# Performance work log

Hardware: AMD Instinct MI355X
Metric: run time of the kernel (lower is better)

Reference implementation:

```python
import jax, jax.numpy as jnp
import numpy as np

P = 100000   # num places
T = 100000   # num transitions
E = 400000   # edges per direction
H = 128      # hidden_dim
L = 3        # num_gnn_layers


def setup_inputs() -> dict:
    key = jax.random.key(0)
    ks = jax.random.split(key, 24)
    w = lambda i, sh: jax.random.normal(ks[i], sh, dtype=jnp.float32) * 0.02
    z = lambda sh: jnp.zeros(sh, dtype=jnp.float32)
    return {
        "place_features": jax.random.uniform(ks[0], (P,), dtype=jnp.float32),
        "transition_features": jax.random.normal(ks[1], (T, 8), dtype=jnp.float32),
        "prefix_encoding": jax.random.normal(ks[2], (18,), dtype=jnp.float32),
        # pre edges: place -> transition ; post edges: transition -> place
        "pre_edge_index": jnp.stack([jax.random.randint(ks[3], (E,), 0, P),
                                     jax.random.randint(ks[4], (E,), 0, T)]).astype(jnp.int32),
        "post_edge_index": jnp.stack([jax.random.randint(ks[5], (E,), 0, T),
                                      jax.random.randint(ks[6], (E,), 0, P)]).astype(jnp.int32),
        # embeddings
        "W_pe": w(7, (1, H)), "b_pe": z((H,)),
        "W_te": w(8, (8, H)), "b_te": z((H,)),
        "W_pr": w(9, (18, H)), "b_pr": z((H,)),
        # per-layer HeteroGraphConv params (stacked over L)
        "p2t_W": w(10, (L, H, H)), "p2t_b": z((L, H)),
        "t2p_W": w(11, (L, H, H)), "t2p_b": z((L, H)),
        "pu_W": w(12, (L, 2 * H, H)), "pu_b": z((L, H)),
        "tu_W": w(13, (L, 2 * H, H)), "tu_b": z((L, H)),
        "pa_W": w(14, (L, H)), "pa_b": z((L,)),
        "ta_W": w(15, (L, H)), "ta_b": z((L,)),
        # pooling + predictor head
        "W_pp": w(16, (H, H)), "b_pp": z((H,)),
        "W_tp": w(17, (H, H)), "b_tp": z((H,)),
        "W1": w(18, (3 * H, 2 * H)), "b1": z((2 * H,)),
        "W2": w(19, (2 * H, H)), "b2": z((H,)),
        "W3": w(20, (H, T)), "b3": z((T,)),
    }


def _forward(place_features, transition_features, prefix_encoding,
             W_pe, b_pe, W_te, b_te, W_pr, b_pr,
             p2t_W, p2t_b, t2p_W, t2p_b, pu_W, pu_b, tu_W, tu_b,
             pa_W, pa_b, ta_W, ta_b,
             W_pp, b_pp, W_tp, b_tp, W1, b1, W2, b2, W3, b3,
             pre_edge_index, post_edge_index):
    place_h = place_features[:, None] @ W_pe + b_pe            # [P,H]
    trans_h = transition_features @ W_te + b_te                # [T,H]
    prefix_h = prefix_encoding[None, :] @ W_pr + b_pr          # [1,H]
    p_src, p_dst = pre_edge_index[0], pre_edge_index[1]        # place idx, trans idx
    t_src, t_dst = post_edge_index[0], post_edge_index[1]      # trans idx, place idx
    nP, nT = place_h.shape[0], trans_h.shape[0]
    for l in range(L):  # fixed small layer count
        # place -> transition: gather, linear, softmax over ALL edges (dim=0 in torch), scatter-add
        m_pt = place_h[p_src] @ p2t_W[l] + p2t_b[l]            # [E,H]
        a_pt = jax.nn.softmax(m_pt @ ta_W[l] + ta_b[l], axis=0)  # [E]
        trans_msg = jax.ops.segment_sum(m_pt * a_pt[:, None], p_dst, num_segments=nT)
        # transition -> place
        m_tp = trans_h[t_src] @ t2p_W[l] + t2p_b[l]            # [E,H]
        a_tp = jax.nn.softmax(m_tp @ pa_W[l] + pa_b[l], axis=0)
        place_msg = jax.ops.segment_sum(m_tp * a_tp[:, None], t_dst, num_segments=nP)
        # residual update + relu (dropout is identity at eval)
        place_new = jnp.concatenate([place_h, place_msg], axis=1) @ pu_W[l] + pu_b[l]
        trans_new = jnp.concatenate([trans_h, trans_msg], axis=1) @ tu_W[l] + tu_b[l]
        place_h = jax.nn.relu(place_h + place_new)
        trans_h = jax.nn.relu(trans_h + trans_new)
    place_global = jnp.mean(place_h @ W_pp + b_pp, axis=0, keepdims=True)   # [1,H]
    trans_global = jnp.mean(trans_h @ W_tp + b_tp, axis=0, keepdims=True)   # [1,H]
    combined = jnp.concatenate([place_global, trans_global, prefix_h], axis=1)  # [1,3H]
    h1 = jax.nn.relu(combined @ W1 + b1)
    h2 = jax.nn.relu(h1 @ W2 + b2)
    logits = h2 @ W3 + b3                                      # [1,T]
    return jax.nn.sigmoid(logits)                              # predicted_transitions


def reference(place_features, transition_features, prefix_encoding,
              pre_edge_index, post_edge_index,
              W_pe, b_pe, W_te, b_te, W_pr, b_pr,
              p2t_W, p2t_b, t2p_W, t2p_b, pu_W, pu_b, tu_W, tu_b,
              pa_W, pa_b, ta_W, ta_b,
              W_pp, b_pp, W_tp, b_tp, W1, b1, W2, b2, W3, b3):
    return _forward(place_features, transition_features, prefix_encoding,
                    W_pe, b_pe, W_te, b_te, W_pr, b_pr,
                    p2t_W, p2t_b, t2p_W, t2p_b, pu_W, pu_b, tu_W, tu_b,
                    pa_W, pa_b, ta_W, ta_b,
                    W_pp, b_pp, W_tp, b_tp, W1, b1, W2, b2, W3, b3,
                    pre_edge_index, post_edge_index)
```

## Files before the change

### kernel.cpp

```cpp
#include <hip/hip_runtime.h>
#include <cstddef>

#define H 128

typedef unsigned short ushort_t;
typedef unsigned char uchar_t;
typedef __attribute__((ext_vector_type(8))) short short8;
typedef __attribute__((ext_vector_type(4))) float floatx4;
typedef __attribute__((ext_vector_type(2))) float floatx2;

__device__ __forceinline__ unsigned fkey(float f){
    unsigned u = __float_as_uint(f);
    return (u & 0x80000000u) ? ~u : (u | 0x80000000u);
}
__device__ __forceinline__ float funkey(unsigned k){
    unsigned u = (k & 0x80000000u) ? (k ^ 0x80000000u) : ~k;
    return __uint_as_float(u);
}
__device__ __forceinline__ ushort_t f2bf(float f){
    unsigned u = __float_as_uint(f);
    u += 0x7fffu + ((u >> 16) & 1u);
    return (ushort_t)(u >> 16);
}
__device__ __forceinline__ float bf2f(ushort_t h){
    return __uint_as_float(((unsigned)h) << 16);
}
__device__ __forceinline__ uchar_t f2fp8(float v){
    int p = __builtin_amdgcn_cvt_pk_fp8_f32(v, v, 0, false);
    return (uchar_t)(p & 0xff);
}
__device__ __forceinline__ void gll16(const void* g, void* l){
    __builtin_amdgcn_global_load_lds(
        (const __attribute__((address_space(1))) unsigned int*)g,
        (__attribute__((address_space(3))) unsigned int*)l, 16, 0, 0);
}
__device__ __forceinline__ void acc8f8(float* a, int2 u, float w){
    floatx2 p;
    p = __builtin_amdgcn_cvt_pk_f32_fp8(u.x, false); a[0] += w*p.x; a[1] += w*p.y;
    p = __builtin_amdgcn_cvt_pk_f32_fp8(u.x, true);  a[2] += w*p.x; a[3] += w*p.y;
    p = __builtin_amdgcn_cvt_pk_f32_fp8(u.y, false); a[4] += w*p.x; a[5] += w*p.y;
    p = __builtin_amdgcn_cvt_pk_f32_fp8(u.y, true);  a[6] += w*p.x; a[7] += w*p.y;
}

__global__ __launch_bounds__(256) void k_embed_place(
    const float* __restrict__ pf, const float* __restrict__ Wpe,
    const float* __restrict__ bpe, ushort_t* __restrict__ out,
    uchar_t* __restrict__ outf8, int P)
{
    int idx = blockIdx.x*256 + threadIdx.x;
    if (idx >= P*32) return;
    int p = idx >> 5, q = (idx & 31) << 2;
    float v = pf[p];
    float4 w = *(const float4*)(Wpe + q);
    float4 b = *(const float4*)(bpe + q);
    float v0 = v*w.x + b.x, v1 = v*w.y + b.y, v2 = v*w.z + b.z, v3 = v*w.w + b.w;
    ushort4 o;
    o.x = f2bf(v0); o.y = f2bf(v1); o.z = f2bf(v2); o.w = f2bf(v3);
    *(ushort4*)(out + (size_t)p*H + q) = o;
    int pk = __builtin_amdgcn_cvt_pk_fp8_f32(v0, v1, 0, false);
    pk = __builtin_amdgcn_cvt_pk_fp8_f32(v2, v3, pk, true);
    *(int*)(outf8 + (size_t)p*H + q) = pk;
}

__global__ __launch_bounds__(256) void k_embed_trans(
    const float* __restrict__ tf, const float* __restrict__ Wte,
    const float* __restrict__ bte, ushort_t* __restrict__ out,
    uchar_t* __restrict__ outf8, int T)
{
    __shared__ float Wl[8*H];
    __shared__ float Bl[H];
    int tid = threadIdx.x;
    #pragma unroll
    for (int t = 0; t < 4; t++) Wl[tid + t*256] = Wte[tid + t*256];
    if (tid < H) Bl[tid] = bte[tid];
    __syncthreads();
    int idx = blockIdx.x*256 + tid;
    if (idx >= T*32) return;
    int t = idx >> 5, q = (idx & 31) << 2;
    float4 acc = *(float4*)(&Bl[q]);
    #pragma unroll
    for (int k = 0; k < 8; k++){
        float s = tf[(size_t)t*8 + k];
        float4 w = *(float4*)(&Wl[k*H + q]);
        acc.x += s*w.x; acc.y += s*w.y; acc.z += s*w.z; acc.w += s*w.w;
    }
    ushort4 o;
    o.x = f2bf(acc.x); o.y = f2bf(acc.y); o.z = f2bf(acc.z); o.w = f2bf(acc.w);
    *(ushort4*)(out + (size_t)t*H + q) = o;
    int pk = __builtin_amdgcn_cvt_pk_fp8_f32(acc.x, acc.y, 0, false);
    pk = __builtin_amdgcn_cvt_pk_fp8_f32(acc.z, acc.w, pk, true);
    *(int*)(outf8 + (size_t)t*H + q) = pk;
}

__global__ void k_init_small(const float* __restrict__ pe, int plen,
                             const float* __restrict__ Wpr, const float* __restrict__ bpr,
                             float* __restrict__ prefix, float* __restrict__ meanP,
                             float* __restrict__ meanT, float* __restrict__ slots)
{
    int c = threadIdx.x;
    float a = bpr[c];
    for (int k = 0; k < plen; k++) a += pe[k]*Wpr[k*H + c];
    prefix[c] = a;
    meanP[c] = 0.f;
    meanT[c] = 0.f;
    if (c < 16) slots[c] = 0.f;
}

__global__ __launch_bounds__(256) void k_wconv(
    const float* __restrict__ tu_W, const float* __restrict__ pu_W,
    ushort_t* __restrict__ WT, int total)
{
    int e = blockIdx.x*256 + threadIdx.x;
    if (e >= total) return;
    int l = e / 32768, oo = e - l*32768;
    int side = oo >> 14, o2 = oo & 16383;
    int n = o2 >> 7, k = o2 & 127;
    const float* Bm = side ? (pu_W + (size_t)l*32768) : (tu_W + (size_t)l*32768);
    WT[(size_t)l*65536 + (size_t)side*32768 + n*256 + k] = f2bf(Bm[(size_t)k*H + n]);
}

__global__ __launch_bounds__(256) void k_wfold(
    const float* __restrict__ p2t_W, const float* __restrict__ t2p_W,
    const float* __restrict__ tu_W,  const float* __restrict__ pu_W,
    ushort_t* __restrict__ WT, int total)
{
    int e = blockIdx.x*256 + threadIdx.x;
    if (e >= total) return;
    int l = e / 32768, oo = e - l*32768;
    int side = oo >> 14, o2 = oo & 16383;
    int n = o2 >> 7, k = o2 & 127;
    const float* A  = side ? (t2p_W + (size_t)l*16384) : (p2t_W + (size_t)l*16384);
    const float* Bm = side ? (pu_W  + (size_t)l*32768) : (tu_W  + (size_t)l*32768);
    const float* Ar = A + (size_t)k*H;
    const float* Bc = Bm + (size_t)128*H + n;
    float s = 0.f;
    #pragma unroll 4
    for (int j = 0; j < 128; j++) s += Ar[j] * Bc[(size_t)j*H];
    WT[(size_t)l*65536 + (size_t)side*32768 + n*256 + 128 + k] = f2bf(s);
}

__global__ __launch_bounds__(128) void k_wsmall(
    const float* __restrict__ p2t_W, const float* __restrict__ t2p_W,
    const float* __restrict__ tu_W,  const float* __restrict__ pu_W,
    const float* __restrict__ p2t_b, const float* __restrict__ t2p_b,
    const float* __restrict__ ta_W,  const float* __restrict__ ta_b,
    const float* __restrict__ pa_W,  const float* __restrict__ pa_b,
    float* __restrict__ wv, float* __restrict__ c0v, float* __restrict__ bcv)
{
    int b = blockIdx.x, l = b >> 1, side = b & 1;
    const float* A  = side ? (t2p_W + (size_t)l*16384) : (p2t_W + (size_t)l*16384);
    const float* Bm = side ? (pu_W  + (size_t)l*32768) : (tu_W  + (size_t)l*32768);
    const float* ab = side ? (t2p_b + (size_t)l*H) : (p2t_b + (size_t)l*H);
    const float* av = side ? (pa_W  + (size_t)l*H) : (ta_W  + (size_t)l*H);
    float asc       = side ? pa_b[l] : ta_b[l];
    int tid = threadIdx.x;
    int o = (l*2 + side)*H;
    float s = 0.f;
    for (int n = 0; n < 128; n++) s += A[(size_t)tid*H + n] * av[n];
    wv[o + tid] = s;
    float s2 = 0.f;
    for (int j = 0; j < 128; j++) s2 += ab[j] * Bm[(size_t)(128+j)*H + tid];
    bcv[o + tid] = s2;
    if (tid == 0){
        float c = 0.f;
        for (int n = 0; n < 128; n++) c += ab[n]*av[n];
        c0v[l*2 + side] = c + asc;
    }
}

__global__ __launch_bounds__(256) void k_zero_ints(int* __restrict__ p, int n)
{
    int i = blockIdx.x*256 + threadIdx.x;
    int stride = gridDim.x*256;
    for (; i < n; i += stride) p[i] = 0;
}

__global__ __launch_bounds__(256) void k_hist2(
    const int* __restrict__ preD, const int* __restrict__ postD, int E,
    int* __restrict__ cntPre, int* __restrict__ cntPost,
    int* __restrict__ rankPre, int* __restrict__ rankPost)
{
    int i = blockIdx.x*256 + threadIdx.x;
    int stride = gridDim.x*256;
    for (; i < E; i += stride){
        rankPre[i] = atomicAdd(&cntPre[preD[i]], 1);
        rankPost[i] = atomicAdd(&cntPost[postD[i]], 1);
    }
}

__global__ __launch_bounds__(256) void k_scan_part(
    const int* __restrict__ cnt, int N, int* __restrict__ bsum)
{
    __shared__ int wsum[4];
    int tid = threadIdx.x, lane = tid & 63, wid = tid >> 6;
    int base = blockIdx.x*1024 + tid*4;
    int4 v = make_int4(0,0,0,0);
    if (base + 3 < N) v = *(const int4*)(cnt + base);
    else {
        if (base+0 < N) v.x = cnt[base+0];
        if (base+1 < N) v.y = cnt[base+1];
        if (base+2 < N) v.z = cnt[base+2];
    }
    int s = v.x + v.y + v.z + v.w;
    #pragma unroll
    for (int o = 1; o < 64; o <<= 1) s += __shfl_xor(s, o);
    if (lane == 0) wsum[wid] = s;
    __syncthreads();
    if (tid == 0) bsum[blockIdx.x] = wsum[0] + wsum[1] + wsum[2] + wsum[3];
}

__global__ __launch_bounds__(256) void k_scan_bsum(int* __restrict__ bsum, int nb)
{
    __shared__ int wsum[4];
    int tid = threadIdx.x, lane = tid & 63, wid = tid >> 6;
    int x = (tid < nb) ? bsum[tid] : 0;
    int inc = x;
    #pragma unroll
    for (int o = 1; o < 64; o <<= 1){
        int u = __shfl_up(inc, o);
        if (lane >= o) inc += u;
    }
    if (lane == 63) wsum[wid] = inc;
    __syncthreads();
    int woff = 0;
    if (wid > 0) woff += wsum[0];
    if (wid > 1) woff += wsum[1];
    if (wid > 2) woff += wsum[2];
    if (tid < nb) bsum[tid] = woff + inc - x;
}

__global__ __launch_bounds__(256) void k_scan_final(
    const int* __restrict__ cnt, int N, const int* __restrict__ bsum,
    int* __restrict__ rp, int E)
{
    __shared__ int wsum[4];
    int tid = threadIdx.x, lane = tid & 63, wid = tid >> 6;
    int base = blockIdx.x*1024 + tid*4;
    int4 v = make_int4(0,0,0,0);
    if (base + 3 < N) v = *(const int4*)(cnt + base);
    else {
        if (base+0 < N) v.x = cnt[base+0];
        if (base+1 < N) v.y = cnt[base+1];
        if (base+2 < N) v.z = cnt[base+2];
    }
    int t0 = v.x, t1 = t0 + v.y, t2 = t1 + v.z, t3 = t2 + v.w;
    int inc = t3;
    #pragma unroll
    for (int o = 1; o < 64; o <<= 1){
        int u = __shfl_up(inc, o);
        if (lane >= o) inc += u;
    }
    if (lane == 63) wsum[wid] = inc;
    __syncthreads();
    int woff = 0;
    if (wid > 0) woff += wsum[0];
    if (wid > 1) woff += wsum[1];
    if (wid > 2) woff += wsum[2];
    int off = bsum[blockIdx.x] + woff + inc - t3;
    if (base+0 < N) rp[base+0] = off;
    if (base+1 < N) rp[base+1] = off + t0;
    if (base+2 < N) rp[base+2] = off + t1;
    if (base+3 < N) rp[base+3] = off + t2;
    if (blockIdx.x == 0 && tid == 0) rp[N] = E;
}

__global__ __launch_bounds__(256) void k_fill2(
    const int* __restrict__ preS, const int* __restrict__ preD,
    const int* __restrict__ postS, const int* __restrict__ postD, int E,
    const int* __restrict__ rpPre, const int* __restrict__ rankPre, int* __restrict__ csrPre,
    const int* __restrict__ rpPost, const int* __restrict__ rankPost, int* __restrict__ csrPost)
{
    int i = blockIdx.x*256 + threadIdx.x;
    int stride = gridDim.x*256;
    for (; i < E; i += stride){
        csrPre[rpPre[preD[i]] + rankPre[i]] = preS[i];
        csrPost[rpPost[postD[i]] + rankPost[i]] = postS[i];
    }
}

__global__ __launch_bounds__(256) void k_gemv2(
    const ushort_t* __restrict__ Ap, int P,
    const ushort_t* __restrict__ At, int T,
    const float* __restrict__ wvA, const float* __restrict__ wvB,
    const float* __restrict__ c0v, int c0iA, int c0iB,
    float* __restrict__ yA, float* __restrict__ yB,
    unsigned* __restrict__ MkA, unsigned* __restrict__ MkB)
{
    __shared__ float wm[4];
    int half = gridDim.x >> 1;
    int side = (blockIdx.x >= half);
    const ushort_t* A = side ? At : Ap;
    int M = side ? T : P;
    const float* wv = side ? wvB : wvA;
    float c0 = c0v[side ? c0iB : c0iA];
    float* y = side ? yB : yA;
    unsigned* Mk = side ? MkB : MkA;
    int b = side ? (blockIdx.x - half) : blockIdx.x;

    int tid = threadIdx.x, lane = tid & 63, wid = tid >> 6;
    int g = tid >> 4, gl = tid & 15;
    float w8[8];
    #pragma unroll
    for (int i = 0; i < 8; i++) w8[i] = wv[gl*8 + i];
    int stride = half*16;
    float lmax = -3.402823466e38f;
    for (int r = b*16 + g; r < M; r += stride){
        short8 u = *(const short8*)(A + (size_t)r*H + gl*8);
        float s = 0.f;
        #pragma unroll
        for (int i = 0; i < 8; i++) s += bf2f((ushort_t)u[i]) * w8[i];
        s += __shfl_xor(s, 1); s += __shfl_xor(s, 2);
        s += __shfl_xor(s, 4); s += __shfl_xor(s, 8);
        s += c0;
        if (gl == 0) y[r] = s;
        lmax = fmaxf(lmax, s);
    }
    #pragma unroll
    for (int o = 1; o < 64; o <<= 1) lmax = fmaxf(lmax, __shfl_xor(lmax, o));
    if (lane == 0) wm[wid] = lmax;
    __syncthreads();
    if (tid == 0){
        float m = fmaxf(fmaxf(wm[0], wm[1]), fmaxf(wm[2], wm[3]));
        atomicMax(Mk, fkey(m));
    }
}

__global__ __launch_bounds__(256) void k_ew2(
    const int* __restrict__ csrPre, const int* __restrict__ csrPost, int E,
    const float* __restrict__ yA, const float* __restrict__ yB,
    const unsigned* __restrict__ MkA, const unsigned* __restrict__ MkB,
    float* __restrict__ ewA, float* __restrict__ ewB,
    float* __restrict__ SpA, float* __restrict__ SpB)
{
    __shared__ float red[4];
    int half = gridDim.x >> 1;
    int side = (blockIdx.x >= half);
    const int* csr = side ? csrPost : csrPre;
    const float* y = side ? yB : yA;
    float Mv = funkey((side ? MkB : MkA)[0]);
    float* ew = side ? ewB : ewA;
    float* Sp = side ? SpB : SpA;
    int b = side ? (blockIdx.x - half) : blockIdx.x;

    int tid = threadIdx.x, lane = tid & 63, wid = tid >> 6;
    int gid = b*256 + tid, stride = half*256;
    float ls = 0.f;
    for (int j = gid; j < E; j += stride){
        float w = expf(y[csr[j]] - Mv);
        ew[j] = w;
        ls += w;
    }
    #pragma unroll
    for (int o = 1; o < 64; o <<= 1) ls += __shfl_xor(ls, o);
    if (lane == 0) red[wid] = ls;
    __syncthreads();
    if (tid == 0) atomicAdd(Sp, red[0] + red[1] + red[2] + red[3]);
}

__global__ __launch_bounds__(256) void k_gather2(
    const int* __restrict__ rpPre, const int* __restrict__ csrPre, int T,
    const int* __restrict__ rpPost, const int* __restrict__ csrPost, int P,
    const float* __restrict__ ewA, const float* __restrict__ ewB,
    const uchar_t* __restrict__ XP, const uchar_t* __restrict__ XT,
    ushort_t* __restrict__ GbA, ushort_t* __restrict__ GbB,
    float* __restrict__ sdegA, float* __restrict__ sdegB)
{
    int nbT = (T + 15) >> 4;
    int side = (blockIdx.x >= nbT);
    const int* rp   = side ? rpPost : rpPre;
    const int* csr  = side ? csrPost : csrPre;
    const float* ew = side ? ewB : ewA;
    const uchar_t* X = side ? XT : XP;
    ushort_t* G     = side ? GbB : GbA;
    float* sdeg     = side ? sdegB : sdegA;
    int Nrow        = side ? P : T;
    int b = side ? (blockIdx.x - nbT) : blockIdx.x;

    int tid = threadIdx.x;
    int g = tid >> 4, gl = tid & 15;
    int r = b*16 + g;
    if (r >= Nrow) return;
    int j0 = rp[r], j1 = rp[r+1];
    const int2* X8 = (const int2*)X;
    float a[8] = {0.f,0.f,0.f,0.f,0.f,0.f,0.f,0.f};
    float se = 0.f;
    int j = j0;
    for (; j + 1 < j1; j += 2){
        int s0 = csr[j], s1 = csr[j+1];
        float e0 = ew[j], e1 = ew[j+1];
        int2 u0 = X8[(size_t)s0*16 + gl];
        int2 u1 = X8[(size_t)s1*16 + gl];
        se += e0 + e1;
        acc8f8(a, u0, e0);
        acc8f8(a, u1, e1);
    }
    if (j < j1){
        int s0 = csr[j];
        float e0 = ew[j];
        int2 u0 = X8[(size_t)s0*16 + gl];
        se += e0;
        acc8f8(a, u0, e0);
    }
    int4 o;
    o.x = (int)((((unsigned)f2bf(a[1])) << 16) | (unsigned)f2bf(a[0]));
    o.y = (int)((((unsigned)f2bf(a[3])) << 16) | (unsigned)f2bf(a[2]));
    o.z = (int)((((unsigned)f2bf(a[5])) << 16) | (unsigned)f2bf(a[4]));
    o.w = (int)((((unsigned)f2bf(a[7])) << 16) | (unsigned)f2bf(a[6]));
    ((int4*)G)[(size_t)r*16 + gl] = o;
    if (gl == 0) sdeg[r] = se;
}

template<bool STORE>
__global__ __launch_bounds__(256, 4) void k_up2(
    ushort_t* trans_h, ushort_t* place_h,
    const ushort_t* __restrict__ GbA, const ushort_t* __restrict__ GbB,
    const ushort_t* __restrict__ WTl,
    const float* __restrict__ tub, const float* __restrict__ pub,
    const float* __restrict__ bcA, const float* __restrict__ bcB,
    const float* __restrict__ sc4,
    const float* __restrict__ sdegA, const float* __restrict__ sdegB,
    uchar_t* __restrict__ XT, uchar_t* __restrict__ XP,
    int T, int P, int gridT, int gridP,
    float* __restrict__ meanT, float* __restrict__ meanP)
{
    __shared__ __align__(16) char As[3*8192];
    __shared__ float csum[H];
    int side = (blockIdx.x >= gridT);
    ushort_t* A1        = side ? place_h : trans_h;
    const ushort_t* A2  = side ? GbB : GbA;
    const ushort_t* WT  = WTl + (side ? 32768 : 0);
    const float* bias   = side ? pub : tub;
    const float* bcp    = side ? bcB : bcA;
    const float* sdeg   = side ? sdegB : sdegA;
    uchar_t* outF8      = side ? XP : XT;
    int M               = side ? P : T;
    int G               = side ? gridP : gridT;
    int t0              = side ? (blockIdx.x - gridT) : blockIdx.x;
    float* colsum       = side ? meanP : meanT;
    float invS = 1.f / (side ? sc4[3] : sc4[1]);

    int tid = threadIdx.x;
    int lane = tid & 63, wid = tid >> 6;
    int quad = lane >> 4, l15 = lane & 15;
    int strip = wid*32;
    short8 bfr1[2][4], bfr2[2][4];
    float bcol[2], bc2[2];
    #pragma unroll
    for (int j = 0; j < 2; j++){
        int col = strip + j*16 + l15;
        #pragma unroll
        for (int kk = 0; kk < 4; kk++){
            bfr1[j][kk] = *(const short8*)(WT + (size_t)col*256 + kk*32 + quad*8);
            bfr2[j][kk] = *(const short8*)(WT + (size_t)col*256 + 128 + kk*32 + quad*8);
        }
        bcol[j] = bias[col];
        bc2[j]  = bcp[col];
    }
    short8 If0, If1;
    #pragma unroll
    for (int e = 0; e < 8; e++){
        int kloc = quad*8 + e;
        If0[e] = (kloc == l15)      ? (short)0x3F80 : (short)0;
        If1[e] = (kloc == l15 + 16) ? (short)0x3F80 : (short)0;
    }
    if constexpr (!STORE){ if (tid < H) csum[tid] = 0.f; }
    float cs[2] = {0.f, 0.f};

    int tiles = (M + 15) >> 4;
    if (t0 >= tiles) return;
    int srow = tid >> 4;
    int su = (tid & 15) ^ srow;
    const ushort_t* g1b = A1 + (size_t)srow*H + su*8;
    const ushort_t* g2b = A2 + (size_t)srow*H + su*8;
    char* AsB = As;

    #define STAGE_UP(bo, t) do { \
        gll16(g1b + (size_t)(t)*(16*H), AsB + (bo) + (wid<<10)); \
        gll16(g2b + (size_t)(t)*(16*H), AsB + (bo) + 4096 + (wid<<10)); \
    } while(0)

    STAGE_UP(0, t0);
    int t1p = t0 + G;
    if (t1p < tiles){
        STAGE_UP(8192, t1p);
        asm volatile("s_waitcnt vmcnt(2)\ns_barrier" ::: "memory");
    } else {
        asm volatile("s_waitcnt vmcnt(0)\ns_barrier" ::: "memory");
    }

    int t = t0, bo = 0;
    for (;;){
        const char* rb = AsB + bo;
        int row0 = t << 4;
        float4 sd4 = *(const float4*)(sdeg + row0 + quad*4);
        float sdv[4] = {sd4.x, sd4.y, sd4.z, sd4.w};
        short8 a1f[4], a2f[4];
        #pragma unroll
        for (int kk = 0; kk < 4; kk++){
            int sw = ((((kk<<2)+quad) ^ l15) << 4);
            a1f[kk] = *(const short8*)(rb + (l15<<8) + sw);
            a2f[kk] = *(const short8*)(rb + 4096 + (l15<<8) + sw);
        }
        short8 ares = *(const short8*)(rb + (l15<<8) + ((((wid<<2)+quad) ^ l15) << 4));
        floatx4 acc1[2], acc2[2];
        acc1[0] = __builtin_amdgcn_mfma_f32_16x16x32_bf16(ares, If0, (floatx4)0.f, 0,0,0);
        acc1[1] = __builtin_amdgcn_mfma_f32_16x16x32_bf16(ares, If1, (floatx4)0.f, 0,0,0);
        acc2[0] = (floatx4)0.f; acc2[1] = (floatx4)0.f;
        #pragma unroll
        for (int j = 0; j < 2; j++){
            #pragma unroll
            for (int kk = 0; kk < 4; kk++)
                acc1[j] = __builtin_amdgcn_mfma_f32_16x16x32_bf16(a1f[kk], bfr1[j][kk], acc1[j], 0,0,0);
            #pragma unroll
            for (int kk = 0; kk < 4; kk++)
                acc2[j] = __builtin_amdgcn_mfma_f32_16x16x32_bf16(a2f[kk], bfr2[j][kk], acc2[j], 0,0,0);
        }
        #pragma unroll
        for (int j = 0; j < 2; j++){
            int col = strip + j*16 + l15;
            #pragma unroll
            for (int rr = 0; rr < 4; rr++){
                int grow = row0 + quad*4 + rr;
                float v = acc1[j][rr] + invS*(acc2[j][rr] + sdv[rr]*bc2[j]) + bcol[j];
                v = fmaxf(v, 0.f);
                if constexpr (STORE){
                    A1[(size_t)grow*H + col] = f2bf(v);
                    outF8[(size_t)grow*H + col] = f2fp8(v);
                } else {
                    cs[j] += v;
                }
            }
        }
        int tn = t + G;
        if (tn >= tiles) break;
        int tnn = tn + G;
        int bo2 = bo + 8192; if (bo2 >= 24576) bo2 = 0;
        int bo3 = bo2 + 8192; if (bo3 >= 24576) bo3 = 0;
        if (tnn < tiles){
            STAGE_UP(bo3, tnn);
            if constexpr (STORE) asm volatile("s_waitcnt vmcnt(19)\ns_barrier" ::: "memory");
            else                 asm volatile("s_waitcnt vmcnt(3)\ns_barrier" ::: "memory");
        } else {
            if constexpr (STORE) asm volatile("s_waitcnt vmcnt(17)\ns_barrier" ::: "memory");
            else                 asm volatile("s_waitcnt vmcnt(1)\ns_barrier" ::: "memory");
        }
        t = tn; bo = bo2;
    }
    #undef STAGE_UP
    if constexpr (!STORE){
        #pragma unroll
        for (int j = 0; j < 2; j++){
            float v = cs[j];
            v += __shfl_xor(v, 16); v += __shfl_xor(v, 32);
            if (quad == 0) atomicAdd(&csum[strip + j*16 + l15], v);
        }
        __syncthreads();
        if (tid < H) atomicAdd(&colsum[tid], csum[tid]);
    }
}

__global__ __launch_bounds__(256) void k_head(
    const float* __restrict__ meanP, const float* __restrict__ meanT,
    float invP, float invT,
    const float* __restrict__ Wpp, const float* __restrict__ bpp,
    const float* __restrict__ Wtp, const float* __restrict__ btp,
    const float* __restrict__ prefix,
    const float* __restrict__ W1, const float* __restrict__ b1,
    const float* __restrict__ W2, const float* __restrict__ b2,
    float* __restrict__ h2g)
{
    __shared__ float comb[384];
    __shared__ float h1s[256];
    int tid = threadIdx.x;
    if (tid < 128){
        float a = bpp[tid];
        for (int k = 0; k < 128; k++) a += meanP[k]*invP*Wpp[k*H + tid];
        comb[tid] = a;
        comb[256 + tid] = prefix[tid];
    } else {
        int c = tid - 128;
        float a = btp[c];
        for (int k = 0; k < 128; k++) a += meanT[k]*invT*Wtp[k*H + c];
        comb[128 + c] = a;
    }
    __syncthreads();
    {
        float a = b1[tid];
        for (int k = 0; k < 384; k++) a += comb[k]*W1[k*256 + tid];
        h1s[tid] = fmaxf(a, 0.f);
    }
    __syncthreads();
    if (tid < 128){
        float a = b2[tid];
        for (int k = 0; k < 256; k++) a += h1s[k]*W2[k*H + tid];
        h2g[tid] = fmaxf(a, 0.f);
    }
}

__global__ __launch_bounds__(256) void k_logits(
    const float* __restrict__ h2g, const float* __restrict__ W3,
    const float* __restrict__ b3, float* __restrict__ out, int T)
{
    __shared__ float h2l[128];
    int tid = threadIdx.x;
    if (tid < 128) h2l[tid] = h2g[tid];
    __syncthreads();
    int t = blockIdx.x*256 + tid;
    if (t >= T) return;
    float a = b3[t];
    #pragma unroll 8
    for (int k = 0; k < 128; k++) a += h2l[k]*W3[(size_t)k*T + t];
    out[t] = 1.f/(1.f + expf(-a));
}

extern "C" void kernel_launch(void* const* d_in, const int* in_sizes, int n_in,
                              void* d_out, int out_size, void* d_ws, size_t ws_size,
                              hipStream_t stream)
{
    (void)n_in; (void)out_size; (void)ws_size;
    const float* pf    = (const float*)d_in[0];
    const float* tf    = (const float*)d_in[1];
    const float* pe    = (const float*)d_in[2];
    const int*   pre   = (const int*)d_in[3];
    const int*   post  = (const int*)d_in[4];
    const float* W_pe  = (const float*)d_in[5];
    const float* b_pe  = (const float*)d_in[6];
    const float* W_te  = (const float*)d_in[7];
    const float* b_te  = (const float*)d_in[8];
    const float* W_pr  = (const float*)d_in[9];
    const float* b_pr  = (const float*)d_in[10];
    const float* p2t_W = (const float*)d_in[11];
    const float* p2t_b = (const float*)d_in[12];
    const float* t2p_W = (const float*)d_in[13];
    const float* t2p_b = (const float*)d_in[14];
    const float* pu_W  = (const float*)d_in[15];
    const float* pu_b  = (const float*)d_in[16];
    const float* tu_W  = (const float*)d_in[17];
    const float* tu_b  = (const float*)d_in[18];
    const float* pa_W  = (const float*)d_in[19];
    const float* pa_b  = (const float*)d_in[20];
    const float* ta_W  = (const float*)d_in[21];
    const float* ta_b  = (const float*)d_in[22];
    const float* W_pp  = (const float*)d_in[23];
    const float* b_pp  = (const float*)d_in[24];
    const float* W_tp  = (const float*)d_in[25];
    const float* b_tp  = (const float*)d_in[26];
    const float* W1    = (const float*)d_in[27];
    const float* b1    = (const float*)d_in[28];
    const float* W2    = (const float*)d_in[29];
    const float* b2    = (const float*)d_in[30];
    const float* W3    = (const float*)d_in[31];
    const float* b3    = (const float*)d_in[32];

    int P = in_sizes[0];
    int T = in_sizes[1] / 8;
    int E = in_sizes[3] / 2;
    int plen = in_sizes[2];
    int L = in_sizes[11] / (H*H);

    float* ws = (float*)d_ws;
    size_t fP = (size_t)P*H, fT = (size_t)T*H;
    size_t fN = (fP > fT) ? fP : fT;
    int   Nmax = (P > T) ? P : T;

    float* yA    = ws;
    float* yB    = yA + Nmax;
    float* sdegA = yB + Nmax;
    float* sdegB = sdegA + Nmax;
    float* sc    = sdegB + Nmax;
    float* meanP   = sc + 16;
    float* meanT   = sc + 144;
    float* prefix  = sc + 272;
    float* h2g     = sc + 400;
    float* wvv  = sc + 544;
    float* c0v  = wvv + (size_t)L*256;
    float* bcv  = c0v + 32;

    ushort_t* bh = (ushort_t*)(bcv + (size_t)L*256);
    ushort_t* place_h = bh;
    ushort_t* trans_h = place_h + fP;
    ushort_t* GbA     = trans_h + fT;
    ushort_t* GbB     = GbA + fN;
    ushort_t* WTb     = GbB + fN;
    uchar_t*  XP      = (uchar_t*)(WTb + (size_t)L*65536);
    uchar_t*  XT      = XP + fP;

    int* iw = (int*)(XT + fT);
    int* cntPre  = iw;
    int* cntPost = cntPre + T;
    int* rpPre   = cntPost + P;
    int* rpPost  = rpPre + (T + 1);
    int* csrPre  = rpPost + (P + 2);
    int* csrPost = csrPre + E;
    int* rankPre = csrPost + E;
    int* rankPost= rankPre + E;
    int* bsumA   = rankPost + E;
    int* bsumB   = bsumA + 256;

    float* ewA = (float*)rankPre;
    float* ewB = (float*)rankPost;

    const int* pre_src  = pre;          const int* pre_dst  = pre + E;
    const int* post_src = post;         const int* post_dst = post + E;

    int wtot = L*32768;
    int nbT = (T + 1023)/1024, nbP = (P + 1023)/1024;

    int tilesP = (P + 15) >> 4, tilesT = (T + 15) >> 4;
    int gridP = (tilesP + 4)/5, gridT = (tilesT + 4)/5;
    int nbTg = (T + 15) >> 4, nbPg = (P + 15) >> 4;

    k_init_small<<<1, 128, 0, stream>>>(pe, plen, W_pr, b_pr, prefix, meanP, meanT, sc);
    k_wconv<<<(wtot + 255)/256, 256, 0, stream>>>(tu_W, pu_W, WTb, wtot);
    k_wfold<<<(wtot + 255)/256, 256, 0, stream>>>(p2t_W, t2p_W, tu_W, pu_W, WTb, wtot);
    k_wsmall<<<L*2, 128, 0, stream>>>(p2t_W, t2p_W, tu_W, pu_W, p2t_b, t2p_b,
                                      ta_W, ta_b, pa_W, pa_b, wvv, c0v, bcv);
    k_zero_ints<<<256, 256, 0, stream>>>(iw, P + T);
    k_hist2<<<2048, 256, 0, stream>>>(pre_dst, post_dst, E,
                                      cntPre, cntPost, rankPre, rankPost);
    k_scan_part<<<nbT, 256, 0, stream>>>(cntPre, T, bsumA);
    k_scan_bsum<<<1, 256, 0, stream>>>(bsumA, nbT);
    k_scan_final<<<nbT, 256, 0, stream>>>(cntPre, T, bsumA, rpPre, E);
    k_scan_part<<<nbP, 256, 0, stream>>>(cntPost, P, bsumB);
    k_scan_bsum<<<1, 256, 0, stream>>>(bsumB, nbP);
    k_scan_final<<<nbP, 256, 0, stream>>>(cntPost, P, bsumB, rpPost, E);
    k_fill2<<<1024, 256, 0, stream>>>(pre_src, pre_dst, post_src, post_dst, E,
                                      rpPre, rankPre, csrPre,
                                      rpPost, rankPost, csrPost);

    k_embed_place<<<(P*32 + 255)/256, 256, 0, stream>>>(pf, W_pe, b_pe, place_h, XP, P);
    k_embed_trans<<<(T*32 + 255)/256, 256, 0, stream>>>(tf, W_te, b_te, trans_h, XT, T);

    for (int l = 0; l < L; l++){
        const ushort_t* WTl = WTb + (size_t)l*65536;
        const float* pub  = pu_b  + (size_t)l*H;
        const float* tub  = tu_b  + (size_t)l*H;
        const float* wvA  = wvv + (size_t)(l*2 + 0)*H;
        const float* wvB  = wvv + (size_t)(l*2 + 1)*H;
        const float* bcA  = bcv + (size_t)(l*2 + 0)*H;
        const float* bcB  = bcv + (size_t)(l*2 + 1)*H;
        unsigned* MkA = (unsigned*)(sc + l*4 + 0);   float* SpA = sc + l*4 + 1;
        unsigned* MkB = (unsigned*)(sc + l*4 + 2);   float* SpB = sc + l*4 + 3;
        int last = (l == L-1);

        k_gemv2<<<1024, 256, 0, stream>>>(place_h, P, trans_h, T, wvA, wvB,
                                          c0v, l*2 + 0, l*2 + 1, yA, yB, MkA, MkB);
        k_ew2<<<1024, 256, 0, stream>>>(csrPre, csrPost, E, yA, yB, MkA, MkB,
                                        ewA, ewB, SpA, SpB);
        k_gather2<<<nbTg + nbPg, 256, 0, stream>>>(rpPre, csrPre, T,
                                                   rpPost, csrPost, P,
                                                   ewA, ewB, XP, XT,
                                                   GbA, GbB, sdegA, sdegB);
        if (last)
            k_up2<false><<<gridT + gridP, 256, 0, stream>>>(
                trans_h, place_h, GbA, GbB, WTl, tub, pub, bcA, bcB,
                sc + l*4, sdegA, sdegB, XT, XP, T, P, gridT, gridP, meanT, meanP);
        else
            k_up2<true><<<gridT + gridP, 256, 0, stream>>>(
                trans_h, place_h, GbA, GbB, WTl, tub, pub, bcA, bcB,
                sc + l*4, sdegA, sdegB, XT, XP, T, P, gridT, gridP, meanT, meanP);
    }

    k_head<<<1, 256, 0, stream>>>(meanP, meanT, 1.f/(float)P, 1.f/(float)T,
                                  W_pp, b_pp, W_tp, b_tp, prefix, W1, b1, W2, b2, h2g);
    k_logits<<<(T + 255)/256, 256, 0, stream>>>(h2g, W3, b3, (float*)d_out, T);
}
```

Before: 684.3 us.

## Shard column-sum atomics, merge weight prep kernels, halve update grid

The final-layer column-sum atomics are spread across 32 sharded accumulators, which k_head reduces before the pooling GEMV. This cuts contention on the 128 global addresses. The weight conversion and fold kernels are merged into one launch. The k_up2 grid is halved so each block handles twice as many 16-row tiles, trading parallelism for fewer blocks and less per-block setup.

```diff
diff --git a/kernel.cpp b/kernel.cpp
--- a/kernel.cpp
+++ b/kernel.cpp
@@ -94,32 +94,18 @@
 
 __global__ void k_init_small(const float* __restrict__ pe, int plen,
                              const float* __restrict__ Wpr, const float* __restrict__ bpr,
-                             float* __restrict__ prefix, float* __restrict__ meanP,
-                             float* __restrict__ meanT, float* __restrict__ slots)
+                             float* __restrict__ prefix, float* __restrict__ meanPsh,
+                             float* __restrict__ meanTsh, float* __restrict__ slots)
 {
     int c = threadIdx.x;
     float a = bpr[c];
     for (int k = 0; k < plen; k++) a += pe[k]*Wpr[k*H + c];
     prefix[c] = a;
-    meanP[c] = 0.f;
-    meanT[c] = 0.f;
+    for (int i = c; i < 4096; i += 128){ meanPsh[i] = 0.f; meanTsh[i] = 0.f; }
     if (c < 16) slots[c] = 0.f;
 }
 
-__global__ __launch_bounds__(256) void k_wconv(
-    const float* __restrict__ tu_W, const float* __restrict__ pu_W,
-    ushort_t* __restrict__ WT, int total)
-{
-    int e = blockIdx.x*256 + threadIdx.x;
-    if (e >= total) return;
-    int l = e / 32768, oo = e - l*32768;
-    int side = oo >> 14, o2 = oo & 16383;
-    int n = o2 >> 7, k = o2 & 127;
-    const float* Bm = side ? (pu_W + (size_t)l*32768) : (tu_W + (size_t)l*32768);
-    WT[(size_t)l*65536 + (size_t)side*32768 + n*256 + k] = f2bf(Bm[(size_t)k*H + n]);
-}
-
-__global__ __launch_bounds__(256) void k_wfold(
+__global__ __launch_bounds__(256) void k_wprep2(
     const float* __restrict__ p2t_W, const float* __restrict__ t2p_W,
     const float* __restrict__ tu_W,  const float* __restrict__ pu_W,
     ushort_t* __restrict__ WT, int total)
@@ -131,12 +117,14 @@
     int n = o2 >> 7, k = o2 & 127;
     const float* A  = side ? (t2p_W + (size_t)l*16384) : (p2t_W + (size_t)l*16384);
     const float* Bm = side ? (pu_W  + (size_t)l*32768) : (tu_W  + (size_t)l*32768);
+    ushort_t* dst = WT + (size_t)l*65536 + (size_t)side*32768 + n*256;
+    dst[k] = f2bf(Bm[(size_t)k*H + n]);
     const float* Ar = A + (size_t)k*H;
     const float* Bc = Bm + (size_t)128*H + n;
     float s = 0.f;
     #pragma unroll 4
     for (int j = 0; j < 128; j++) s += Ar[j] * Bc[(size_t)j*H];
-    WT[(size_t)l*65536 + (size_t)side*32768 + n*256 + 128 + k] = f2bf(s);
+    dst[128 + k] = f2bf(s);
 }
 
 __global__ __launch_bounds__(128) void k_wsmall(
@@ -421,7 +409,7 @@
     const float* __restrict__ sdegA, const float* __restrict__ sdegB,
     uchar_t* __restrict__ XT, uchar_t* __restrict__ XP,
     int T, int P, int gridT, int gridP,
-    float* __restrict__ meanT, float* __restrict__ meanP)
+    float* __restrict__ meanTsh, float* __restrict__ meanPsh)
 {
     __shared__ __align__(16) char As[3*8192];
     __shared__ float csum[H];
@@ -436,7 +424,7 @@
     int M               = side ? P : T;
     int G               = side ? gridP : gridT;
     int t0              = side ? (blockIdx.x - gridT) : blockIdx.x;
-    float* colsum       = side ? meanP : meanT;
+    float* colsum       = side ? meanPsh : meanTsh;
     float invS = 1.f / (side ? sc4[3] : sc4[1]);
 
     int tid = threadIdx.x;
@@ -555,12 +543,12 @@
             if (quad == 0) atomicAdd(&csum[strip + j*16 + l15], v);
         }
         __syncthreads();
-        if (tid < H) atomicAdd(&colsum[tid], csum[tid]);
+        if (tid < H) atomicAdd(&colsum[((blockIdx.x & 31) << 7) + tid], csum[tid]);
     }
 }
 
 __global__ __launch_bounds__(256) void k_head(
-    const float* __restrict__ meanP, const float* __restrict__ meanT,
+    const float* __restrict__ meanPsh, const float* __restrict__ meanTsh,
     float invP, float invT,
     const float* __restrict__ Wpp, const float* __restrict__ bpp,
     const float* __restrict__ Wtp, const float* __restrict__ btp,
@@ -569,18 +557,30 @@
     const float* __restrict__ W2, const float* __restrict__ b2,
     float* __restrict__ h2g)
 {
+    __shared__ float mp[128], mt[128];
     __shared__ float comb[384];
     __shared__ float h1s[256];
     int tid = threadIdx.x;
     if (tid < 128){
+        float s = 0.f;
+        for (int c = 0; c < 32; c++) s += meanPsh[(c << 7) + tid];
+        mp[tid] = s;
+    } else {
+        int c2 = tid - 128;
+        float s = 0.f;
+        for (int c = 0; c < 32; c++) s += meanTsh[(c << 7) + c2];
+        mt[c2] = s;
+    }
+    __syncthreads();
+    if (tid < 128){
         float a = bpp[tid];
-        for (int k = 0; k < 128; k++) a += meanP[k]*invP*Wpp[k*H + tid];
+        for (int k = 0; k < 128; k++) a += mp[k]*invP*Wpp[k*H + tid];
         comb[tid] = a;
         comb[256 + tid] = prefix[tid];
     } else {
         int c = tid - 128;
         float a = btp[c];
-        for (int k = 0; k < 128; k++) a += meanT[k]*invT*Wtp[k*H + c];
+        for (int k = 0; k < 128; k++) a += mt[k]*invT*Wtp[k*H + c];
         comb[128 + c] = a;
     }
     __syncthreads();
@@ -668,11 +668,11 @@
     float* sdegA = yB + Nmax;
     float* sdegB = sdegA + Nmax;
     float* sc    = sdegB + Nmax;
-    float* meanP   = sc + 16;
-    float* meanT   = sc + 144;
-    float* prefix  = sc + 272;
-    float* h2g     = sc + 400;
-    float* wvv  = sc + 544;
+    float* meanPsh = sc + 16;
+    float* meanTsh = meanPsh + 4096;
+    float* prefix  = meanTsh + 4096;
+    float* h2g     = prefix + 128;
+    float* wvv  = h2g + 128;
     float* c0v  = wvv + (size_t)L*256;
     float* bcv  = c0v + 32;
 
@@ -707,12 +707,12 @@
     int nbT = (T + 1023)/1024, nbP = (P + 1023)/1024;
 
     int tilesP = (P + 15) >> 4, tilesT = (T + 15) >> 4;
-    int gridP = (tilesP + 4)/5, gridT = (tilesT + 4)/5;
+    int gridP = (tilesP + 9)/10, gridT = (tilesT + 9)/10;
     int nbTg = (T + 15) >> 4, nbPg = (P + 15) >> 4;
 
-    k_init_small<<<1, 128, 0, stream>>>(pe, plen, W_pr, b_pr, prefix, meanP, meanT, sc);
-    k_wconv<<<(wtot + 255)/256, 256, 0, stream>>>(tu_W, pu_W, WTb, wtot);
-    k_wfold<<<(wtot + 255)/256, 256, 0, stream>>>(p2t_W, t2p_W, tu_W, pu_W, WTb, wtot);
+    k_init_small<<<1, 128, 0, stream>>>(pe, plen, W_pr, b_pr, prefix,
+                                        meanPsh, meanTsh, sc);
+    k_wprep2<<<(wtot + 255)/256, 256, 0, stream>>>(p2t_W, t2p_W, tu_W, pu_W, WTb, wtot);
     k_wsmall<<<L*2, 128, 0, stream>>>(p2t_W, t2p_W, tu_W, pu_W, p2t_b, t2p_b,
                                       ta_W, ta_b, pa_W, pa_b, wvv, c0v, bcv);
     k_zero_ints<<<256, 256, 0, stream>>>(iw, P + T);
@@ -754,14 +754,16 @@
         if (last)
             k_up2<false><<<gridT + gridP, 256, 0, stream>>>(
                 trans_h, place_h, GbA, GbB, WTl, tub, pub, bcA, bcB,
-                sc + l*4, sdegA, sdegB, XT, XP, T, P, gridT, gridP, meanT, meanP);
+                sc + l*4, sdegA, sdegB, XT, XP, T, P, gridT, gridP,
+                meanTsh, meanPsh);
         else
             k_up2<true><<<gridT + gridP, 256, 0, stream>>>(
                 trans_h, place_h, GbA, GbB, WTl, tub, pub, bcA, bcB,
-                sc + l*4, sdegA, sdegB, XT, XP, T, P, gridT, gridP, meanT, meanP);
-    }
-
-    k_head<<<1, 256, 0, stream>>>(meanP, meanT, 1.f/(float)P, 1.f/(float)T,
+                sc + l*4, sdegA, sdegB, XT, XP, T, P, gridT, gridP,
+                meanTsh, meanPsh);
+    }
+
+    k_head<<<1, 256, 0, stream>>>(meanPsh, meanTsh, 1.f/(float)P, 1.f/(float)T,
                                   W_pp, b_pp, W_tp, b_tp, prefix, W1, b1, W2, b2, h2g);
     k_logits<<<(T + 255)/256, 256, 0, stream>>>(h2g, W3, b3, (float*)d_out, T);
 }
```

Measured after the change: 657.4 us. 3.9% less time.
